# Kernel optimization log

Hardware: AMD Instinct MI355X
Metric: run time of the kernel (lower is better)

The kernel has to match this reference:

```python
import jax, jax.numpy as jnp
import numpy as np

N = 2048; E = 5; C = 2

def _gtconv(A, w):
    # softmax over edge types; original uses weight[i,j].item() -> detached scalar
    s = jax.nn.softmax(w, axis=1)                       # [C, E]
    sd = jax.lax.stop_gradient(s)
    # concat + coalesce(op='add') of scaled edge lists == weighted sum of adjacencies
    comb = jnp.einsum('ce,enm->cnm', sd, A)             # [C, N, N]
    return comb, s

def _normalize(H):
    # scatter_add of edge values over rows == row sums; D^{-1/2} row scaling
    deg = jnp.sum(H, axis=-1)                           # [C, N]
    dinv = deg ** -0.5
    dinv = jnp.where(jnp.isinf(dinv), 0.0, dinv)
    return dinv[:, :, None] * H

def setup_inputs() -> dict:
    key = jax.random.key(0)
    ks = jax.random.split(key, 10)
    vals = jax.random.uniform(ks[0], (E, N, N), dtype=jnp.float32)
    mask = jax.random.uniform(ks[1], (E, N, N)) < 0.01
    A = jnp.where(mask, vals, 0.0)
    X = jax.random.normal(ks[2], (N, 512), dtype=jnp.float32)
    w0_1 = jax.random.normal(ks[3], (C, E), dtype=jnp.float32)
    w0_2 = jax.random.normal(ks[4], (C, E), dtype=jnp.float32)
    w1_1 = jax.random.normal(ks[5], (C, E), dtype=jnp.float32)
    gcn_w = jax.random.normal(ks[6], (128, 512), dtype=jnp.float32) * 0.04
    gcn_b = jnp.zeros((128,), jnp.float32)
    lin_w = jax.random.normal(ks[7], (8, C * 128), dtype=jnp.float32) * 0.06
    lin_b = jnp.zeros((8,), jnp.float32)
    target_x = jax.random.randint(ks[8], (512,), 0, N)
    return {"A": A, "X": X, "w0_1": w0_1, "w0_2": w0_2, "w1_1": w1_1,
            "gcn_w": gcn_w, "gcn_b": gcn_b, "lin_w": lin_w, "lin_b": lin_b,
            "target_x": target_x}

def reference(A, X, w0_1, w0_2, w1_1, gcn_w, gcn_b, lin_w, lin_b, target_x):
    # ---- layer 0 (first=True): two GTConvs, SpGEMM A1 @ A2 per channel ----
    HA, s1 = _gtconv(A, w0_1)
    HB, s2 = _gtconv(A, w0_2)
    H = jnp.einsum('cij,cjk->cik', HA, HB)              # [C, N, N]
    H = _normalize(H)
    # ---- layer 1 (first=False): H @ conv1(A) ----
    HB2, s3 = _gtconv(A, w1_1)
    H = jnp.einsum('cij,cjk->cik', H, HB2)
    H = _normalize(H)
    all_Ws = jnp.stack([s1, s2, s3])                    # [3, C, E]
    # ---- node classification head (H is not used in feature prop, as in source) ----
    x = jax.nn.relu(X @ gcn_w.T + gcn_b)                # [N, w_out]
    X_ = jnp.concatenate([x] * C, axis=1)               # [N, C*w_out]
    y = X_[target_x] @ lin_w.T + lin_b                  # [T, num_class]
    return (y, all_Ws, H)
```

## Files before the change

### kernel.cpp

```cpp
#include <hip/hip_runtime.h>
#include <hip/hip_fp8.h>
#include <stdint.h>

#define N2 2048
#define NN (2048UL * 2048UL)

typedef __attribute__((ext_vector_type(4))) float f32x4;
typedef __attribute__((ext_vector_type(4))) int   i32x4;
typedef __attribute__((ext_vector_type(8))) int   i32x8;

__device__ __forceinline__ unsigned char f2f8(float x) {
    __hip_fp8_e4m3 t(x);
    return t.__x;
}
__device__ __forceinline__ float f82f(unsigned char b) {
    __hip_fp8_e4m3 t;
    t.__x = b;
    return (float)t;
}

__device__ __forceinline__ unsigned f2f8x4(const float* a) {
#if __has_builtin(__builtin_amdgcn_cvt_pk_fp8_f32)
    int w = 0;
    w = __builtin_amdgcn_cvt_pk_fp8_f32(a[0], a[1], w, false);
    w = __builtin_amdgcn_cvt_pk_fp8_f32(a[2], a[3], w, true);
    return (unsigned)w;
#else
    union { unsigned char b[4]; unsigned v; } o;
    #pragma unroll
    for (int i = 0; i < 4; i++) o.b[i] = f2f8(a[i]);
    return o.v;
#endif
}
__device__ __forceinline__ uint2 f2f8x8(const float* a) {
    uint2 r; r.x = f2f8x4(a); r.y = f2f8x4(a + 4);
    return r;
}

__device__ __forceinline__ void gload16(const void* g, void* l) {
    __builtin_amdgcn_global_load_lds(
        (const __attribute__((address_space(1))) unsigned int*)g,
        (__attribute__((address_space(3))) unsigned int*)l, 16, 0, 0);
}

__global__ __launch_bounds__(512, 8) void combine_kernel(
    const float* __restrict__ A, const float* __restrict__ w01,
    const float* __restrict__ w02, const float* __restrict__ w11,
    unsigned char* __restrict__ HA, unsigned char* __restrict__ HBt,
    unsigned char* __restrict__ HB2t, float* __restrict__ PB2) {
    __shared__ float s[3][2][5];
    __shared__ float tile[2][64][33];
    const int tid = threadIdx.x;
    if (tid < 6) {
        const int wi = tid >> 1, c = tid & 1;
        const float* w = (wi == 0 ? w01 : (wi == 1 ? w02 : w11)) + c * 5;
        float mx = w[0];
        for (int e = 1; e < 5; e++) mx = fmaxf(mx, w[e]);
        float ex[5], sum = 0.f;
        for (int e = 0; e < 5; e++) { ex[e] = expf(w[e] - mx); sum += ex[e]; }
        for (int e = 0; e < 5; e++) s[wi][c][e] = ex[e] / sum;
    }
    __syncthreads();

    const int nr  = tid >> 4;
    const int mc4 = (tid & 15) * 4;
    const size_t gn = (size_t)blockIdx.y * 32 + nr;
    const size_t gm = (size_t)blockIdx.x * 64 + mc4;
    const float* ap = A + gn * N2 + gm;

    float4 av[5];
    #pragma unroll
    for (int e = 0; e < 5; e++) av[e] = *(const float4*)(ap + (size_t)e * NN);

    float acc[6][4] = {};
    #pragma unroll
    for (int e = 0; e < 5; e++) {
        const float a[4] = {av[e].x, av[e].y, av[e].z, av[e].w};
        #pragma unroll
        for (int c = 0; c < 2; c++) {
            const float q0 = s[0][c][e], q1 = s[1][c][e], q2 = s[2][c][e];
            #pragma unroll
            for (int i = 0; i < 4; i++) {
                acc[c][i]     += q0 * a[i];
                acc[2 + c][i] += q1 * a[i];
                acc[4 + c][i] += q2 * a[i];
            }
        }
    }

    #pragma unroll
    for (int c = 0; c < 2; c++)
        *(unsigned*)&HA[(size_t)c * NN + gn * N2 + gm] = f2f8x4(acc[c]);

    #pragma unroll
    for (int c = 0; c < 2; c++) {
        float v = acc[4 + c][0] + acc[4 + c][1] + acc[4 + c][2] + acc[4 + c][3];
        v += __shfl_xor(v, 1);
        v += __shfl_xor(v, 2);
        v += __shfl_xor(v, 4);
        v += __shfl_xor(v, 8);
        if ((tid & 15) == 0)
            PB2[(size_t)c * 32 * 2048 + (size_t)blockIdx.x * 2048 + gn] = v;
    }

    #pragma unroll
    for (int rr = 0; rr < 2; rr++) {
        __syncthreads();
        #pragma unroll
        for (int rl = 0; rl < 2; rl++)
            #pragma unroll
            for (int i = 0; i < 4; i++)
                tile[rl][mc4 + i][nr] = acc[2 + rr * 2 + rl][i];
        __syncthreads();
        {
            const int ch   = tid >> 8;
            const int mrow = (tid >> 2) & 63;
            const int ns   = (tid & 3) * 8;
            float a[8];
            const float4 t0 = *(const float4*)&tile[ch][mrow][ns];
            const float4 t1 = *(const float4*)&tile[ch][mrow][ns + 4];
            a[0] = t0.x; a[1] = t0.y; a[2] = t0.z; a[3] = t0.w;
            a[4] = t1.x; a[5] = t1.y; a[6] = t1.z; a[7] = t1.w;
            unsigned char* dst = (rr == 0 ? HBt : HB2t) + (size_t)ch * NN
                + ((size_t)blockIdx.x * 64 + mrow) * N2
                + (size_t)blockIdx.y * 32 + ns;
            *(uint2*)dst = f2f8x8(a);
        }
    }
}

__global__ __launch_bounds__(256) void b2fold_kernel(
    const float* __restrict__ PB2, float* __restrict__ b2sum) {
    const int r = blockIdx.x * 256 + threadIdx.x;
    const int c = r >> 11, n = r & 2047;
    float sum = 0.f;
    #pragma unroll
    for (int bx = 0; bx < 32; bx++) sum += PB2[c * 65536 + bx * 2048 + n];
    b2sum[r] = sum;
}

#define GBM 256
#define GBN 128
#define GBK 128
#define BUF_BYTES 49152
#define B_OFF 32768
#define SCALE1 0x7F7F7F7F

template <int MODE>
__global__ __launch_bounds__(512, 2) void gemm_mx(
    const unsigned char* __restrict__ A, const unsigned char* __restrict__ Bt,
    void* __restrict__ Cout, float* __restrict__ P,
    const float* __restrict__ sfac) {
    __shared__ unsigned char lds[3 * BUF_BYTES];

    const int tid  = threadIdx.x;
    const int wave = tid >> 6, lane = tid & 63;
    const int wm = wave >> 1, wn = wave & 1;
    const int wr = wm * 64;
    const int wc = wn * 64;
    const int l16 = lane & 15, lhi = lane >> 4;

    const int brow = blockIdx.y * GBM;
    const int bcol = blockIdx.x * GBN;
    const size_t cz = (size_t)blockIdx.z * NN;
    const unsigned char* Ab  = A  + cz + (size_t)brow * N2;
    const unsigned char* Btb = Bt + cz + (size_t)bcol * N2;

    const unsigned char* src[6];
    #pragma unroll
    for (int L = 0; L < 4; L++) {
        const int g = L * 512 + tid;
        const int r = g >> 3, s = (g & 7) ^ (r & 7);
        src[L] = Ab + (size_t)r * N2 + s * 16;
    }
    #pragma unroll
    for (int L = 4; L < 6; L++) {
        const int h = (L - 4) * 512 + tid;
        const int r = h >> 3, s = (h & 7) ^ (r & 7);
        src[L] = Btb + (size_t)r * N2 + s * 16;
    }

    #define STAGE6(buf, k0)                                                   \
        do {                                                                  \
            unsigned char* dst = lds + (buf) * BUF_BYTES + tid * 16;          \
            _Pragma("unroll")                                                 \
            for (int i = 0; i < 6; i++)                                       \
                gload16(src[i] + (k0), dst + i * 8192);                       \
        } while (0)

    f32x4 acc[4][4] = {};

    STAGE6(0, 0);
    STAGE6(1, GBK);

    const int nt = N2 / GBK;
    for (int t = 0; t < nt; ++t) {
        const unsigned char* base = lds + (t % 3) * BUF_BYTES;

        if (t < nt - 1) asm volatile("s_waitcnt vmcnt(6)" ::: "memory");
        else            asm volatile("s_waitcnt vmcnt(0)" ::: "memory");
        __builtin_amdgcn_s_barrier();
        __builtin_amdgcn_sched_barrier(0);

        i32x8 af0[2], bfr[4], af1[2];
        #pragma unroll
        for (int m = 0; m < 2; m++) {
            const int row = wr + m * 16 + l16;
            const unsigned char* rp = base + row * 128;
            const i32x4 lo = *(const i32x4*)(rp + (((2 * lhi)     ^ (row & 7)) * 16));
            const i32x4 hi = *(const i32x4*)(rp + (((2 * lhi + 1) ^ (row & 7)) * 16));
            #pragma unroll
            for (int q = 0; q < 4; q++) { af0[m][q] = lo[q]; af0[m][4 + q] = hi[q]; }
        }
        #pragma unroll
        for (int n = 0; n < 4; n++) {
            const int row = wc + n * 16 + l16;
            const unsigned char* rp = base + B_OFF + row * 128;
            const i32x4 lo = *(const i32x4*)(rp + (((2 * lhi)     ^ (row & 7)) * 16));
            const i32x4 hi = *(const i32x4*)(rp + (((2 * lhi + 1) ^ (row & 7)) * 16));
            #pragma unroll
            for (int q = 0; q < 4; q++) { bfr[n][q] = lo[q]; bfr[n][4 + q] = hi[q]; }
        }
        #pragma unroll
        for (int m = 0; m < 2; m++) {
            const int row = wr + 32 + m * 16 + l16;
            const unsigned char* rp = base + row * 128;
            const i32x4 lo = *(const i32x4*)(rp + (((2 * lhi)     ^ (row & 7)) * 16));
            const i32x4 hi = *(const i32x4*)(rp + (((2 * lhi + 1) ^ (row & 7)) * 16));
            #pragma unroll
            for (int q = 0; q < 4; q++) { af1[m][q] = lo[q]; af1[m][4 + q] = hi[q]; }
        }
        if (t + 2 < nt) STAGE6((t + 2) % 3, (t + 2) * GBK);

        __builtin_amdgcn_s_setprio(1);
        #pragma unroll
        for (int m = 0; m < 2; m++)
            #pragma unroll
            for (int n = 0; n < 4; n++)
                acc[m][n] = __builtin_amdgcn_mfma_scale_f32_16x16x128_f8f6f4(
                    af0[m], bfr[n], acc[m][n], 0, 0, 0, SCALE1, 0, SCALE1);
        #pragma unroll
        for (int m = 0; m < 2; m++)
            #pragma unroll
            for (int n = 0; n < 4; n++)
                acc[2 + m][n] = __builtin_amdgcn_mfma_scale_f32_16x16x128_f8f6f4(
                    af1[m], bfr[n], acc[2 + m][n], 0, 0, 0, SCALE1, 0, SCALE1);
        __builtin_amdgcn_s_setprio(0);
    }
    #undef STAGE6

    if constexpr (MODE == 0) {
        unsigned char* Cb = (unsigned char*)Cout + cz + (size_t)brow * N2 + bcol;
        #pragma unroll
        for (int m = 0; m < 4; m++) {
            const int r0 = wr + m * 16 + lhi * 4;
            #pragma unroll
            for (int n = 0; n < 4; n++) {
                const int c0 = wc + n * 16 + l16;
                #pragma unroll
                for (int j = 0; j < 4; j++)
                    Cb[(size_t)(r0 + j) * N2 + c0] = f2f8(acc[m][n][j]);
            }
        }
        const size_t pb = (size_t)(blockIdx.x * 2 + wn) * 4096
                        + (size_t)blockIdx.z * 2048 + brow + wr;
        #pragma unroll
        for (int m = 0; m < 4; m++)
            #pragma unroll
            for (int j = 0; j < 4; j++) {
                float ps = acc[m][0][j] + acc[m][1][j] + acc[m][2][j] + acc[m][3][j];
                ps += __shfl_xor(ps, 1);
                ps += __shfl_xor(ps, 2);
                ps += __shfl_xor(ps, 4);
                ps += __shfl_xor(ps, 8);
                if (l16 == 0) P[pb + m * 16 + lhi * 4 + j] = ps;
            }
    } else {
        float* Cb = (float*)Cout + cz + (size_t)brow * N2 + bcol;
        float sf[4][4];
        #pragma unroll
        for (int m = 0; m < 4; m++)
            #pragma unroll
            for (int j = 0; j < 4; j++)
                sf[m][j] = sfac[blockIdx.z * 2048 + brow + wr + m * 16 + lhi * 4 + j];
        #pragma unroll
        for (int m = 0; m < 4; m++) {
            const int r0 = wr + m * 16 + lhi * 4;
            #pragma unroll
            for (int n = 0; n < 4; n++) {
                const int c0 = wc + n * 16 + l16;
                #pragma unroll
                for (int j = 0; j < 4; j++)
                    Cb[(size_t)(r0 + j) * N2 + c0] = acc[m][n][j] * sf[m][j];
            }
        }
    }
}

__device__ __forceinline__ float block_sum256(float v) {
    #pragma unroll
    for (int off = 32; off; off >>= 1) v += __shfl_xor(v, off, 64);
    __shared__ float wsum[4];
    if ((threadIdx.x & 63) == 0) wsum[threadIdx.x >> 6] = v;
    __syncthreads();
    return wsum[0] + wsum[1] + wsum[2] + wsum[3];
}

__global__ __launch_bounds__(256) void gemv_sfac_kernel(
    const unsigned char* __restrict__ C0, const float* __restrict__ b2sum,
    const float* __restrict__ P, float* __restrict__ sfac) {
    const size_t r = blockIdx.x;
    const int tid = threadIdx.x;

    float s0 = 0.f;
    if (tid < 64) {
        float v = P[(size_t)(tid & 31) * 4096 + r];
        v += __shfl_xor(v, 1);
        v += __shfl_xor(v, 2);
        v += __shfl_xor(v, 4);
        v += __shfl_xor(v, 8);
        v += __shfl_xor(v, 16);
        s0 = v;
    }

    const unsigned char* row = C0 + r * N2;
    const float* bs = b2sum + ((r >> 11) << 11);
    const int base = tid * 8;
    union { uint2 v; unsigned char b[8]; } u;
    u.v = *(const uint2*)&row[base];
    float sum = 0.f;
    #pragma unroll
    for (int i = 0; i < 8; i++) sum += f82f(u.b[i]) * bs[base + i];
    const float tot = block_sum256(sum);
    if (tid == 0) {
        const float d0 = s0 > 0.f ? rsqrtf(s0) : 0.f;
        const float deg1 = d0 * tot;
        sfac[r] = d0 * (deg1 > 0.f ? rsqrtf(deg1) : 0.f);
    }
}

__global__ __launch_bounds__(256) void head_kernel(
    const float* __restrict__ X, const float* __restrict__ gcn_w,
    const float* __restrict__ gcn_b, const float* __restrict__ lin_w,
    const float* __restrict__ lin_b, const int* __restrict__ tx,
    const float* __restrict__ w01, const float* __restrict__ w02,
    const float* __restrict__ w11,
    float* __restrict__ y, float* __restrict__ allw) {
    __shared__ float xr[8][512];
    __shared__ float xk[8][132];
    __shared__ int trg[8];
    const int tid = threadIdx.x, b = blockIdx.x;
    if (tid < 8) trg[tid] = tx[b * 8 + tid];
    __syncthreads();
    #pragma unroll
    for (int q = 0; q < 4; q++) {
        const int idx = q * 1024 + tid * 4;
        const int t = idx >> 9, col = idx & 511;
        *(float4*)&xr[t][col] = *(const float4*)&X[(size_t)trg[t] * 512 + col];
    }
    __syncthreads();
    const int k = tid & 127, tp = tid >> 7;
    const float* wrp = gcn_w + (size_t)k * 512;
    float d[4] = {0.f, 0.f, 0.f, 0.f};
    for (int i = 0; i < 512; i += 4) {
        const float4 wv = *(const float4*)&wrp[i];
        #pragma unroll
        for (int tt = 0; tt < 4; tt++) {
            const float* xp = xr[tp * 4 + tt];
            d[tt] += xp[i] * wv.x + xp[i+1] * wv.y + xp[i+2] * wv.z + xp[i+3] * wv.w;
        }
    }
    const float gb = gcn_b[k];
    #pragma unroll
    for (int tt = 0; tt < 4; tt++) xk[tp * 4 + tt][k] = fmaxf(d[tt] + gb, 0.f);
    __syncthreads();
    if (tid < 64) {
        const int t = tid >> 3, o = tid & 7;
        float a = lin_b[o];
        const float* lw = lin_w + o * 256;
        for (int kk = 0; kk < 128; kk++)
            a += xk[t][kk] * (lw[kk] + lw[128 + kk]);
        y[(size_t)(b * 8 + t) * 8 + o] = a;
    }
    if (b == 0 && tid >= 64 && tid < 70) {
        const int t6 = tid - 64;
        const int wi = t6 >> 1, c = t6 & 1;
        const float* w = (wi == 0 ? w01 : (wi == 1 ? w02 : w11)) + c * 5;
        float mx = w[0];
        for (int e = 1; e < 5; e++) mx = fmaxf(mx, w[e]);
        float ex[5], sum = 0.f;
        for (int e = 0; e < 5; e++) { ex[e] = expf(w[e] - mx); sum += ex[e]; }
        for (int e = 0; e < 5; e++) allw[t6 * 5 + e] = ex[e] / sum;
    }
}

extern "C" void kernel_launch(void* const* d_in, const int* in_sizes, int n_in,
                              void* d_out, int out_size, void* d_ws, size_t ws_size,
                              hipStream_t stream) {
    const float* A     = (const float*)d_in[0];
    const float* X     = (const float*)d_in[1];
    const float* w01   = (const float*)d_in[2];
    const float* w02   = (const float*)d_in[3];
    const float* w11   = (const float*)d_in[4];
    const float* gcn_w = (const float*)d_in[5];
    const float* gcn_b = (const float*)d_in[6];
    const float* lin_w = (const float*)d_in[7];
    const float* lin_b = (const float*)d_in[8];
    const int*   tx    = (const int*)d_in[9];

    float* out  = (float*)d_out;
    float* y    = out;
    float* allw = out + 4096;
    float* H    = out + 4126;

    unsigned char* HA   = (unsigned char*)d_ws;
    unsigned char* HBt  = HA + 2 * NN;
    unsigned char* HB2t = HBt + 2 * NN;
    unsigned char* C0   = HB2t + 2 * NN;
    float* P     = (float*)(C0 + 2 * NN);
    float* PB2   = P + 32 * 4096;
    float* b2sum = PB2 + 2 * 32 * 2048;
    float* sfac  = b2sum + 4096;

    combine_kernel<<<dim3(32, 64), 512, 0, stream>>>(A, w01, w02, w11,
                                                     HA, HBt, HB2t, PB2);
    b2fold_kernel<<<16, 256, 0, stream>>>(PB2, b2sum);
    gemm_mx<0><<<dim3(16, 8, 2), 512, 0, stream>>>(HA, HBt, C0, P, nullptr);
    gemv_sfac_kernel<<<4096, 256, 0, stream>>>(C0, b2sum, P, sfac);
    gemm_mx<1><<<dim3(16, 8, 2), 512, 0, stream>>>(C0, HB2t, H, nullptr, sfac);
    head_kernel<<<64, 256, 0, stream>>>(X, gcn_w, gcn_b, lin_w, lin_b, tx,
                                        w01, w02, w11, y, allw);
}
```

Baseline: 103.1 us.

## Shrink FP8 GEMM tile to 128x128 with 256 threads and double buffering

The block tile of both MX-FP8 GEMMs drops from 256x128 to 128x128 with 4 waves instead of 8, and the grid doubles to 512 blocks. Each wave now covers 64 rows and loads four A fragments at once. The triple-buffered LDS pipeline is replaced by double buffering, where the prefetch of tile t+2 is issued after the MFMAs behind an extra barrier. The aim is more blocks per CU and smaller LDS use for better latency hiding, at the cost of less data reuse per block and one more barrier per K step.

```diff
diff --git a/kernel.cpp b/kernel.cpp
--- a/kernel.cpp
+++ b/kernel.cpp
@@ -139,19 +139,19 @@
     b2sum[r] = sum;
 }
 
-#define GBM 256
+#define GBM 128
 #define GBN 128
 #define GBK 128
-#define BUF_BYTES 49152
-#define B_OFF 32768
+#define BUF_BYTES 32768
+#define B_OFF 16384
 #define SCALE1 0x7F7F7F7F
 
 template <int MODE>
-__global__ __launch_bounds__(512, 2) void gemm_mx(
+__global__ __launch_bounds__(256, 2) void gemm_mx(
     const unsigned char* __restrict__ A, const unsigned char* __restrict__ Bt,
     void* __restrict__ Cout, float* __restrict__ P,
     const float* __restrict__ sfac) {
-    __shared__ unsigned char lds[3 * BUF_BYTES];
+    __shared__ unsigned char lds[2 * BUF_BYTES];
 
     const int tid  = threadIdx.x;
     const int wave = tid >> 6, lane = tid & 63;
@@ -166,51 +166,51 @@
     const unsigned char* Ab  = A  + cz + (size_t)brow * N2;
     const unsigned char* Btb = Bt + cz + (size_t)bcol * N2;
 
-    const unsigned char* src[6];
+    const unsigned char* src[8];
     #pragma unroll
     for (int L = 0; L < 4; L++) {
-        const int g = L * 512 + tid;
+        const int g = L * 256 + tid;
         const int r = g >> 3, s = (g & 7) ^ (r & 7);
         src[L] = Ab + (size_t)r * N2 + s * 16;
     }
     #pragma unroll
-    for (int L = 4; L < 6; L++) {
-        const int h = (L - 4) * 512 + tid;
+    for (int L = 4; L < 8; L++) {
+        const int h = (L - 4) * 256 + tid;
         const int r = h >> 3, s = (h & 7) ^ (r & 7);
         src[L] = Btb + (size_t)r * N2 + s * 16;
     }
 
-    #define STAGE6(buf, k0)                                                   \
+    #define STAGE8(buf, k0)                                                   \
         do {                                                                  \
             unsigned char* dst = lds + (buf) * BUF_BYTES + tid * 16;          \
             _Pragma("unroll")                                                 \
-            for (int i = 0; i < 6; i++)                                       \
-                gload16(src[i] + (k0), dst + i * 8192);                       \
+            for (int i = 0; i < 8; i++)                                       \
+                gload16(src[i] + (k0), dst + i * 4096);                       \
         } while (0)
 
     f32x4 acc[4][4] = {};
 
-    STAGE6(0, 0);
-    STAGE6(1, GBK);
+    STAGE8(0, 0);
+    STAGE8(1, GBK);
 
     const int nt = N2 / GBK;
     for (int t = 0; t < nt; ++t) {
-        const unsigned char* base = lds + (t % 3) * BUF_BYTES;
-
-        if (t < nt - 1) asm volatile("s_waitcnt vmcnt(6)" ::: "memory");
+        const unsigned char* base = lds + (t & 1) * BUF_BYTES;
+
+        if (t < nt - 1) asm volatile("s_waitcnt vmcnt(8)" ::: "memory");
         else            asm volatile("s_waitcnt vmcnt(0)" ::: "memory");
         __builtin_amdgcn_s_barrier();
         __builtin_amdgcn_sched_barrier(0);
 
-        i32x8 af0[2], bfr[4], af1[2];
-        #pragma unroll
-        for (int m = 0; m < 2; m++) {
+        i32x8 af[4], bfr[4];
+        #pragma unroll
+        for (int m = 0; m < 4; m++) {
             const int row = wr + m * 16 + l16;
             const unsigned char* rp = base + row * 128;
             const i32x4 lo = *(const i32x4*)(rp + (((2 * lhi)     ^ (row & 7)) * 16));
             const i32x4 hi = *(const i32x4*)(rp + (((2 * lhi + 1) ^ (row & 7)) * 16));
             #pragma unroll
-            for (int q = 0; q < 4; q++) { af0[m][q] = lo[q]; af0[m][4 + q] = hi[q]; }
+            for (int q = 0; q < 4; q++) { af[m][q] = lo[q]; af[m][4 + q] = hi[q]; }
         }
         #pragma unroll
         for (int n = 0; n < 4; n++) {
@@ -221,33 +221,22 @@
             #pragma unroll
             for (int q = 0; q < 4; q++) { bfr[n][q] = lo[q]; bfr[n][4 + q] = hi[q]; }
         }
-        #pragma unroll
-        for (int m = 0; m < 2; m++) {
-            const int row = wr + 32 + m * 16 + l16;
-            const unsigned char* rp = base + row * 128;
-            const i32x4 lo = *(const i32x4*)(rp + (((2 * lhi)     ^ (row & 7)) * 16));
-            const i32x4 hi = *(const i32x4*)(rp + (((2 * lhi + 1) ^ (row & 7)) * 16));
-            #pragma unroll
-            for (int q = 0; q < 4; q++) { af1[m][q] = lo[q]; af1[m][4 + q] = hi[q]; }
-        }
-        if (t + 2 < nt) STAGE6((t + 2) % 3, (t + 2) * GBK);
 
         __builtin_amdgcn_s_setprio(1);
         #pragma unroll
-        for (int m = 0; m < 2; m++)
+        for (int m = 0; m < 4; m++)
             #pragma unroll
             for (int n = 0; n < 4; n++)
                 acc[m][n] = __builtin_amdgcn_mfma_scale_f32_16x16x128_f8f6f4(
-                    af0[m], bfr[n], acc[m][n], 0, 0, 0, SCALE1, 0, SCALE1);
-        #pragma unroll
-        for (int m = 0; m < 2; m++)
-            #pragma unroll
-            for (int n = 0; n < 4; n++)
-                acc[2 + m][n] = __builtin_amdgcn_mfma_scale_f32_16x16x128_f8f6f4(
-                    af1[m], bfr[n], acc[2 + m][n], 0, 0, 0, SCALE1, 0, SCALE1);
+                    af[m], bfr[n], acc[m][n], 0, 0, 0, SCALE1, 0, SCALE1);
         __builtin_amdgcn_s_setprio(0);
-    }
-    #undef STAGE6
+
+        __builtin_amdgcn_sched_barrier(0);
+        __builtin_amdgcn_s_barrier();
+        __builtin_amdgcn_sched_barrier(0);
+        if (t + 2 < nt) STAGE8(t & 1, (t + 2) * GBK);
+    }
+    #undef STAGE8
 
     if constexpr (MODE == 0) {
         unsigned char* Cb = (unsigned char*)Cout + cz + (size_t)brow * N2 + bcol;
@@ -425,9 +414,9 @@
     combine_kernel<<<dim3(32, 64), 512, 0, stream>>>(A, w01, w02, w11,
                                                      HA, HBt, HB2t, PB2);
     b2fold_kernel<<<16, 256, 0, stream>>>(PB2, b2sum);
-    gemm_mx<0><<<dim3(16, 8, 2), 512, 0, stream>>>(HA, HBt, C0, P, nullptr);
+    gemm_mx<0><<<dim3(16, 16, 2), 256, 0, stream>>>(HA, HBt, C0, P, nullptr);
     gemv_sfac_kernel<<<4096, 256, 0, stream>>>(C0, b2sum, P, sfac);
-    gemm_mx<1><<<dim3(16, 8, 2), 512, 0, stream>>>(C0, HB2t, H, nullptr, sfac);
+    gemm_mx<1><<<dim3(16, 16, 2), 256, 0, stream>>>(C0, HB2t, H, nullptr, sfac);
     head_kernel<<<64, 256, 0, stream>>>(X, gcn_w, gcn_b, lin_w, lin_b, tx,
                                         w01, w02, w11, y, allw);
 }
```

New measurement: 100.5 us. 1.03x faster.
